# Kernel tuning notes

Hardware: AMD Instinct MI355X
Metric: run time of the kernel (lower is better)

## Reference

```python
import jax, jax.numpy as jnp
import numpy as np

RELU_NEG_SLOPE = 0.2

def _gat_layer(x, W, a, src, dst, num_nodes, concat):
    # x: [N, Din]; W: [H, Din, F]; a: [H, 2F]; src/dst: [E]
    H, _, F = W.shape
    proj = jnp.einsum('nd,hdf->nhf', x, W)              # [N, H, F]
    a_self, a_nb = a[:, :F], a[:, F:]                   # [H, F] each
    alpha_self = jnp.einsum('nhf,hf->nh', proj, a_self) # [N, H]
    alpha_nb = jnp.einsum('nhf,hf->nh', proj, a_nb)     # [N, H]
    # edge score: a . [proj_dst || proj_src], dst = center node i, src = neighbor j
    e = jax.nn.leaky_relu(alpha_self[dst] + alpha_nb[src], RELU_NEG_SLOPE)  # [E, H]
    e_max = jax.ops.segment_max(e, dst, num_segments=num_nodes)
    e_exp = jnp.exp(e - e_max[dst])
    denom = jax.ops.segment_sum(e_exp, dst, num_segments=num_nodes)
    w = e_exp / denom[dst]                              # [E, H] softmax per dst node
    msg = proj[src] * w[:, :, None]                     # [E, H, F]
    out = jax.ops.segment_sum(msg, dst, num_segments=num_nodes)  # [N, H, F]
    if concat:
        return out.reshape(num_nodes, H * F)
    return out.mean(axis=1)


def setup_inputs() -> dict:
    key = jax.random.key(0)
    k1, k2, k3, k4, k5, k6 = jax.random.split(key, 6)
    N, Din, F1, H1 = 10000, 128, 64, 8
    Dmid = H1 * F1  # 512
    F2, H2 = 64, 1
    x = jax.random.normal(k1, (N, Din), dtype=jnp.float32)
    edges = jax.random.randint(k2, (2, 80000), 0, N, dtype=jnp.int64)
    W1 = jax.random.normal(k3, (H1, Din, F1), dtype=jnp.float32) / np.sqrt(Din)
    a1 = jax.random.normal(k4, (H1, 2 * F1), dtype=jnp.float32) / np.sqrt(2 * F1)
    W2 = jax.random.normal(k5, (H2, Dmid, F2), dtype=jnp.float32) / np.sqrt(Dmid)
    a2 = jax.random.normal(k6, (H2, 2 * F2), dtype=jnp.float32) / np.sqrt(2 * F2)
    return {"x": x, "edges": edges, "W1": W1, "a1": a1, "W2": W2, "a2": a2}


def reference(x, edges, W1, a1, W2, a2):
    N = x.shape[0]
    loops = jnp.arange(N, dtype=edges.dtype)
    # undirected graph + self loops (Graph.neighborhood adds both directions and self)
    src = jnp.concatenate([edges[0], edges[1], loops])
    dst = jnp.concatenate([edges[1], edges[0], loops])
    h = _gat_layer(x, W1, a1, src, dst, N, concat=True)   # [N, 512]
    h = jax.nn.elu(h)
    out = _gat_layer(h, W2, a2, src, dst, N, concat=False)  # [N, 64]
    return out
```

## Files before the change

kernel.cpp:

```cpp
#include <hip/hip_runtime.h>
#include <hip/hip_bf16.h>
#include <hip/hip_fp16.h>

#define RELU_NEG_SLOPE 0.2f

typedef _Float16 half8 __attribute__((ext_vector_type(8)));
typedef float f32x4 __attribute__((ext_vector_type(4)));

__device__ __forceinline__ float leaky(float e) {
    return (e > 0.f) ? e : RELU_NEG_SLOPE * e;
}

__device__ __forceinline__ float elu1(float x) {
    return (x > 0.f) ? x : (__expf(x) - 1.f);
}

__global__ __launch_bounds__(256) void stage_kernel(
    const float4* __restrict__ x4, const float* __restrict__ W1,
    const float* __restrict__ W2, float2* __restrict__ xh,
    __half* __restrict__ Bt1, __half* __restrict__ W2t,
    int* __restrict__ cnt, int n4, int t1, int t2, int N) {
    int i = blockIdx.x * 256 + threadIdx.x;
    if (i < n4) {
        float4 v = x4[i];
        float2 p;
        ((__half2*)&p)[0] = __floats2half2_rn(v.x, v.y);
        ((__half2*)&p)[1] = __floats2half2_rn(v.z, v.w);
        xh[i] = p;
    } else if (i < n4 + t1) {
        int j = i - n4;
        int f = j & 63;
        int d = (j >> 6) & 127;
        int h = j >> 13;
        Bt1[((h * 64 + f) << 7) + d] = __float2half(W1[j]);
    } else if (i < n4 + t1 + t2) {
        int j = i - n4 - t1;
        int f = j & 63;
        int d = j >> 6;
        W2t[f * 512 + d] = __float2half(W2[j]);
    } else if (i < n4 + t1 + t2 + N) {
        cnt[i - n4 - t1 - t2] = 0;
    }
}

__global__ __launch_bounds__(256) void scatter_gemm1(
    const int* __restrict__ edges, int E0, int* __restrict__ cnt,
    unsigned short* __restrict__ ell, int nscat,
    const __half* __restrict__ Ah, const __half* __restrict__ Bt,
    const float* __restrict__ a1, __half* __restrict__ Cp,
    float* __restrict__ as_, float* __restrict__ an_, int M, int slabN) {
    if (blockIdx.x < nscat) {
        int i = blockIdx.x * 256 + threadIdx.x;
        if (i >= 2 * E0) return;
        int s = edges[i];
        int d = (i < E0) ? edges[E0 + i] : edges[i - E0];
        int pos = atomicAdd(&cnt[d], 1);
        ell[(d << 6) + pos] = (unsigned short)s;
        return;
    }
    int bid2 = blockIdx.x - nscat;
    const int h = bid2 & 7;
    const int by = bid2 >> 3;
    const int lane = threadIdx.x & 63;
    const int wave = threadIdx.x >> 6;
    const int q = lane >> 4;
    const int l15 = lane & 15;
    const int mrow = by * 64 + wave * 16;

    f32x4 acc[4] = {{0.f, 0.f, 0.f, 0.f}, {0.f, 0.f, 0.f, 0.f},
                    {0.f, 0.f, 0.f, 0.f}, {0.f, 0.f, 0.f, 0.f}};
    const __half* Ap = Ah + (size_t)(mrow + l15) * 128 + q * 8;
    const __half* Bp = Bt + (size_t)(h * 64 + l15) * 128 + q * 8;
#pragma unroll
    for (int ks = 0; ks < 4; ks++) {
        half8 av = *(const half8*)(Ap + ks * 32);
#pragma unroll
        for (int t = 0; t < 4; t++) {
            half8 bv = *(const half8*)(Bp + (size_t)t * 16 * 128 + ks * 32);
            acc[t] = __builtin_amdgcn_mfma_f32_16x16x32_f16(av, bv, acc[t], 0, 0, 0);
        }
    }

    __half* Cs = Cp + (size_t)(h >> 1) * slabN + (h & 1) * 64;
    float asc[4], anc[4];
#pragma unroll
    for (int t = 0; t < 4; t++) {
        asc[t] = a1[h * 128 + t * 16 + l15];
        anc[t] = a1[h * 128 + 64 + t * 16 + l15];
    }
#pragma unroll
    for (int r = 0; r < 4; r++) {
        int mg = mrow + q * 4 + r;
        float ps = 0.f, pn = 0.f;
#pragma unroll
        for (int t = 0; t < 4; t++) {
            float v = acc[t][r];
            ps += v * asc[t];
            pn += v * anc[t];
            if (mg < M)
                Cs[(size_t)mg * 128 + t * 16 + l15] = __float2half(v);
        }
#pragma unroll
        for (int m = 8; m >= 1; m >>= 1) {
            ps += __shfl_xor(ps, m, 64);
            pn += __shfl_xor(pn, m, 64);
        }
        if (l15 == 0 && mg < M) {
            as_[mg * 8 + h] = ps;
            an_[mg * 8 + h] = pn;
        }
    }
}

__global__ __launch_bounds__(256) void agg_h8_sliced(
    const int* __restrict__ cnt, const unsigned short* __restrict__ ell,
    const __half* __restrict__ projp, const float* __restrict__ as_,
    const float* __restrict__ an_, __half* __restrict__ outh,
    int N, int slabN) {
    int bid = blockIdx.x;
    int hp = bid & 3;
    int rem = bid >> 2;
    int d = rem * 4 + (threadIdx.x >> 6);
    int lane = threadIdx.x & 63;
    if (d >= N) return;
    const int sub = lane >> 3;
    const int inner = lane & 7;
    const int hh = inner >> 2;
    const int h = hp * 2 + hh;
    const int c16 = (inner & 3) * 16;

    int deg = cnt[d];
    const unsigned short* row = ell + (d << 6);
    float asd = as_[d * 8 + h];
    const __half* slab = projp + (size_t)hp * slabN;

    float acc[16];
#pragma unroll
    for (int i = 0; i < 16; i++) acc[i] = 0.f;
    float den = 0.f;
    if (sub == 0) {
        float e = __expf(leaky(asd + an_[d * 8 + h]));
        const __half* p = slab + (size_t)d * 128 + hh * 64 + c16;
        half8 v0 = *(const half8*)p;
        half8 v1 = *(const half8*)(p + 8);
        den = e;
#pragma unroll
        for (int i = 0; i < 8; i++) {
            acc[i] = e * (float)v0[i];
            acc[8 + i] = e * (float)v1[i];
        }
    }
    for (int j0 = 0; j0 < deg; j0 += 8) {
        int j = j0 + sub;
        int jc = (j < deg) ? j : (deg - 1);
        int s = row[jc];
        float e = __expf(leaky(asd + an_[s * 8 + h]));
        if (j >= deg) e = 0.f;
        const __half* p = slab + (size_t)s * 128 + hh * 64 + c16;
        half8 v0 = *(const half8*)p;
        half8 v1 = *(const half8*)(p + 8);
        den += e;
#pragma unroll
        for (int i = 0; i < 8; i++) {
            acc[i] += e * (float)v0[i];
            acc[8 + i] += e * (float)v1[i];
        }
    }

#pragma unroll
    for (int off = 32; off >= 8; off >>= 1) {
#pragma unroll
        for (int i = 0; i < 16; i++) acc[i] += __shfl_down(acc[i], off, 64);
        den += __shfl_down(den, off, 64);
    }

    if (sub == 0) {
        float r = 1.f / den;
        half8 o0, o1;
#pragma unroll
        for (int i = 0; i < 8; i++) {
            o0[i] = (_Float16)elu1(acc[i] * r);
            o1[i] = (_Float16)elu1(acc[8 + i] * r);
        }
        __half* op = outh + (size_t)d * 512 + h * 64 + c16;
        *(half8*)op = o0;
        *(half8*)(op + 8) = o1;
    }
}

__global__ __launch_bounds__(64) void mfma_gemm2(
    const __half* __restrict__ Ah, const __half* __restrict__ Bt,
    const float* __restrict__ a2, __half* __restrict__ Ch,
    float* __restrict__ as_, float* __restrict__ an_, int M) {
    const int lane = threadIdx.x & 63;
    const int q = lane >> 4;
    const int l15 = lane & 15;
    const int mrow = blockIdx.x * 16;

    f32x4 acc[4] = {{0.f, 0.f, 0.f, 0.f}, {0.f, 0.f, 0.f, 0.f},
                    {0.f, 0.f, 0.f, 0.f}, {0.f, 0.f, 0.f, 0.f}};
    const __half* Ap = Ah + (size_t)(mrow + l15) * 512 + q * 8;
    const __half* Bp = Bt + (size_t)l15 * 512 + q * 8;
#pragma unroll
    for (int ks = 0; ks < 16; ks++) {
        half8 av = *(const half8*)(Ap + ks * 32);
#pragma unroll
        for (int t = 0; t < 4; t++) {
            half8 bv = *(const half8*)(Bp + (size_t)t * 16 * 512 + ks * 32);
            acc[t] = __builtin_amdgcn_mfma_f32_16x16x32_f16(av, bv, acc[t], 0, 0, 0);
        }
    }

    float asc[4], anc[4];
#pragma unroll
    for (int t = 0; t < 4; t++) {
        asc[t] = a2[t * 16 + l15];
        anc[t] = a2[64 + t * 16 + l15];
    }
#pragma unroll
    for (int r = 0; r < 4; r++) {
        int mg = mrow + q * 4 + r;
        float ps = 0.f, pn = 0.f;
#pragma unroll
        for (int t = 0; t < 4; t++) {
            float v = acc[t][r];
            ps += v * asc[t];
            pn += v * anc[t];
            if (mg < M)
                Ch[(size_t)mg * 64 + t * 16 + l15] = __float2half(v);
        }
#pragma unroll
        for (int m = 8; m >= 1; m >>= 1) {
            ps += __shfl_xor(ps, m, 64);
            pn += __shfl_xor(pn, m, 64);
        }
        if (l15 == 0 && mg < M) {
            as_[mg] = ps;
            an_[mg] = pn;
        }
    }
}

__global__ __launch_bounds__(256) void agg_node_h1(
    const int* __restrict__ cnt, const unsigned short* __restrict__ ell,
    const __half* __restrict__ projh, const float* __restrict__ as_,
    const float* __restrict__ an_, float* __restrict__ out, int N) {
    int d = blockIdx.x * 4 + (threadIdx.x >> 6);
    int lane = threadIdx.x & 63;
    if (d >= N) return;
    int sub = lane >> 3;
    int inner = lane & 7;
    int deg = cnt[d];
    const unsigned short* row = ell + (d << 6);
    float asd = as_[d];

    float acc[8];
#pragma unroll
    for (int i = 0; i < 8; i++) acc[i] = 0.f;
    float den = 0.f;
    for (int j0 = 0; j0 < deg; j0 += 8) {
        int j = j0 + sub;
        int jc = (j < deg) ? j : (deg - 1);
        int s = row[jc];
        float e = __expf(leaky(asd + an_[s]));
        if (j >= deg) e = 0.f;
        half8 v = *(const half8*)(projh + (size_t)s * 64 + inner * 8);
        den += e;
#pragma unroll
        for (int i = 0; i < 8; i++) acc[i] += e * (float)v[i];
    }

#pragma unroll
    for (int off = 32; off >= 8; off >>= 1) {
#pragma unroll
        for (int i = 0; i < 8; i++) acc[i] += __shfl_down(acc[i], off, 64);
        den += __shfl_down(den, off, 64);
    }

    if (sub == 0) {
        float e = __expf(leaky(asd + an_[d]));
        half8 v = *(const half8*)(projh + (size_t)d * 64 + inner * 8);
        den += e;
#pragma unroll
        for (int i = 0; i < 8; i++) acc[i] += e * (float)v[i];
        float rden = 1.f / den;
        float4 r0, r1;
        r0.x = acc[0] * rden; r0.y = acc[1] * rden;
        r0.z = acc[2] * rden; r0.w = acc[3] * rden;
        r1.x = acc[4] * rden; r1.y = acc[5] * rden;
        r1.z = acc[6] * rden; r1.w = acc[7] * rden;
        float* op = out + (size_t)d * 64 + inner * 8;
        *(float4*)op = r0;
        *(float4*)(op + 4) = r1;
    }
}

extern "C" void kernel_launch(void* const* d_in, const int* in_sizes, int n_in,
                              void* d_out, int out_size, void* d_ws, size_t ws_size,
                              hipStream_t stream) {
    const float* x  = (const float*)d_in[0];
    const int* edges = (const int*)d_in[1];
    const float* W1 = (const float*)d_in[2];
    const float* a1 = (const float*)d_in[3];
    const float* W2 = (const float*)d_in[4];
    const float* a2 = (const float*)d_in[5];

    const int Din = 128, H1 = 8, F = 64, Dmid = 512;
    const int N = in_sizes[0] / Din;
    const int E0 = in_sizes[1] / 2;
    const int Mpad = (N + 63) & ~63;
    const int slabN = Mpad * 128;

    char* base = (char*)d_ws;
    size_t off = 0;
    auto take = [&](size_t bytes) {
        void* p = base + off;
        off = (off + bytes + 255) & ~(size_t)255;
        return p;
    };
    __half* x_h    = (__half*)take((size_t)Mpad * Din * 2);
    __half* proj1p = (__half*)take((size_t)4 * slabN * 2);
    __half* hbufh  = (__half*)take((size_t)Mpad * Dmid * 2);
    __half* proj2h = (__half*)take((size_t)N * F * 2);
    __half* Bt1    = (__half*)take((size_t)Dmid * Din * 2);
    __half* W2t    = (__half*)take((size_t)F * Dmid * 2);
    float* as1 = (float*)take((size_t)N * H1 * 4);
    float* an1 = (float*)take((size_t)N * H1 * 4);
    float* as2 = (float*)take((size_t)N * 4);
    float* an2 = (float*)take((size_t)N * 4);
    int* cnt = (int*)take((size_t)N * 4);
    unsigned short* ell = (unsigned short*)take((size_t)N * 64 * 2);

    int n4 = N * Din / 4;
    int t1 = H1 * Din * F, t2 = Dmid * F;
    int total = n4 + t1 + t2 + N;
    stage_kernel<<<(total + 255) / 256, 256, 0, stream>>>(
        (const float4*)x, W1, W2, (float2*)x_h, Bt1, W2t, cnt, n4, t1, t2, N);

    int nscat = (2 * E0 + 255) / 256;
    int ngemm = H1 * ((N + 63) / 64);
    scatter_gemm1<<<nscat + ngemm, 256, 0, stream>>>(
        edges, E0, cnt, ell, nscat,
        x_h, Bt1, a1, proj1p, as1, an1, N, slabN);

    int nbp = (N + 3) / 4;
    agg_h8_sliced<<<4 * nbp, 256, 0, stream>>>(cnt, ell, proj1p, as1, an1,
                                               hbufh, N, slabN);

    mfma_gemm2<<<(N + 15) / 16, 64, 0, stream>>>(hbufh, W2t, a2, proj2h,
                                                 as2, an2, N);

    agg_node_h1<<<(N + 3) / 4, 256, 0, stream>>>(cnt, ell, proj2h,
                                                 as2, an2, (float*)d_out, N);
}
```

Before: 140.9 us.

## Fuse all GAT stages into one cooperative persistent kernel with grid syncs

Merges the five separate kernel launches (stage, scatter+gemm1, agg1, gemm2, agg2) into one cooperative persistent kernel. The stages are separated by grid-wide barriers, and each stage's work is distributed with grid-stride loops over blocks or waves. The aim is to remove per-launch overhead and the gaps between kernels. In exchange, occupancy is capped at a fixed grid size of up to 1024 blocks, grid syncs have their own cost, and the standalone kernels remain as a fallback if the cooperative launch fails.

Result: slower. 439.6 us (+211.9%).

```diff
diff --git a/kernel.cpp b/kernel.cpp
--- a/kernel.cpp
+++ b/kernel.cpp
@@ -1,6 +1,8 @@
 #include <hip/hip_runtime.h>
-#include <hip/hip_bf16.h>
 #include <hip/hip_fp16.h>
+#include <hip/hip_cooperative_groups.h>
+
+namespace cg = cooperative_groups;
 
 #define RELU_NEG_SLOPE 0.2f
 
@@ -15,62 +17,68 @@
     return (x > 0.f) ? x : (__expf(x) - 1.f);
 }
 
-__global__ __launch_bounds__(256) void stage_kernel(
-    const float4* __restrict__ x4, const float* __restrict__ W1,
-    const float* __restrict__ W2, float2* __restrict__ xh,
-    __half* __restrict__ Bt1, __half* __restrict__ W2t,
-    int* __restrict__ cnt, int n4, int t1, int t2, int N) {
-    int i = blockIdx.x * 256 + threadIdx.x;
-    if (i < n4) {
-        float4 v = x4[i];
-        float2 p;
-        ((__half2*)&p)[0] = __floats2half2_rn(v.x, v.y);
-        ((__half2*)&p)[1] = __floats2half2_rn(v.z, v.w);
-        xh[i] = p;
-    } else if (i < n4 + t1) {
-        int j = i - n4;
+struct GatParams {
+    const float4* __restrict__ x4;
+    const float* __restrict__ W1;
+    const float* __restrict__ W2;
+    const float* __restrict__ a1;
+    const float* __restrict__ a2;
+    const int* __restrict__ edges;
+    float2* __restrict__ xh;
+    __half* __restrict__ Bt1;
+    __half* __restrict__ W2t;
+    int* __restrict__ cnt;
+    unsigned short* __restrict__ ell;
+    __half* __restrict__ proj1p;
+    float* __restrict__ as1;
+    float* __restrict__ an1;
+    __half* __restrict__ hbufh;
+    __half* __restrict__ proj2h;
+    float* __restrict__ as2;
+    float* __restrict__ an2;
+    float* __restrict__ out;
+    int N, E0, n4, t1, t2, slabN, ntiles1, ntiles2;
+};
+
+
+__device__ __forceinline__ void stage_item(const GatParams& p, int i) {
+    if (i < p.n4) {
+        float4 v = p.x4[i];
+        float2 o;
+        ((__half2*)&o)[0] = __floats2half2_rn(v.x, v.y);
+        ((__half2*)&o)[1] = __floats2half2_rn(v.z, v.w);
+        p.xh[i] = o;
+    } else if (i < p.n4 + p.t1) {
+        int j = i - p.n4;
         int f = j & 63;
         int d = (j >> 6) & 127;
         int h = j >> 13;
-        Bt1[((h * 64 + f) << 7) + d] = __float2half(W1[j]);
-    } else if (i < n4 + t1 + t2) {
-        int j = i - n4 - t1;
+        p.Bt1[((h * 64 + f) << 7) + d] = __float2half(p.W1[j]);
+    } else if (i < p.n4 + p.t1 + p.t2) {
+        int j = i - p.n4 - p.t1;
         int f = j & 63;
         int d = j >> 6;
-        W2t[f * 512 + d] = __float2half(W2[j]);
-    } else if (i < n4 + t1 + t2 + N) {
-        cnt[i - n4 - t1 - t2] = 0;
-    }
-}
-
-__global__ __launch_bounds__(256) void scatter_gemm1(
-    const int* __restrict__ edges, int E0, int* __restrict__ cnt,
-    unsigned short* __restrict__ ell, int nscat,
-    const __half* __restrict__ Ah, const __half* __restrict__ Bt,
-    const float* __restrict__ a1, __half* __restrict__ Cp,
-    float* __restrict__ as_, float* __restrict__ an_, int M, int slabN) {
-    if (blockIdx.x < nscat) {
-        int i = blockIdx.x * 256 + threadIdx.x;
-        if (i >= 2 * E0) return;
-        int s = edges[i];
-        int d = (i < E0) ? edges[E0 + i] : edges[i - E0];
-        int pos = atomicAdd(&cnt[d], 1);
-        ell[(d << 6) + pos] = (unsigned short)s;
-        return;
-    }
-    int bid2 = blockIdx.x - nscat;
-    const int h = bid2 & 7;
-    const int by = bid2 >> 3;
-    const int lane = threadIdx.x & 63;
-    const int wave = threadIdx.x >> 6;
+        p.W2t[f * 512 + d] = __float2half(p.W2[j]);
+    } else {
+        p.cnt[i - p.n4 - p.t1 - p.t2] = 0;
+    }
+}
+
+__device__ __forceinline__ void scatter_item(const GatParams& p, int i) {
+    int s = p.edges[i];
+    int d = (i < p.E0) ? p.edges[p.E0 + i] : p.edges[i - p.E0];
+    int pos = atomicAdd(&p.cnt[d], 1);
+    p.ell[(d << 6) + pos] = (unsigned short)s;
+}
+
+__device__ __forceinline__ void gemm1_wave(const GatParams& p, int h,
+                                           int mrow, int lane) {
     const int q = lane >> 4;
     const int l15 = lane & 15;
-    const int mrow = by * 64 + wave * 16;
-
     f32x4 acc[4] = {{0.f, 0.f, 0.f, 0.f}, {0.f, 0.f, 0.f, 0.f},
                     {0.f, 0.f, 0.f, 0.f}, {0.f, 0.f, 0.f, 0.f}};
-    const __half* Ap = Ah + (size_t)(mrow + l15) * 128 + q * 8;
-    const __half* Bp = Bt + (size_t)(h * 64 + l15) * 128 + q * 8;
+    const __half* Ap = (const __half*)p.xh + (size_t)(mrow + l15) * 128 + q * 8;
+    const __half* Bp = p.Bt1 + (size_t)(h * 64 + l15) * 128 + q * 8;
 #pragma unroll
     for (int ks = 0; ks < 4; ks++) {
         half8 av = *(const half8*)(Ap + ks * 32);
@@ -80,13 +88,12 @@
             acc[t] = __builtin_amdgcn_mfma_f32_16x16x32_f16(av, bv, acc[t], 0, 0, 0);
         }
     }
-
-    __half* Cs = Cp + (size_t)(h >> 1) * slabN + (h & 1) * 64;
+    __half* Cs = p.proj1p + (size_t)(h >> 1) * p.slabN + (h & 1) * 64;
     float asc[4], anc[4];
 #pragma unroll
     for (int t = 0; t < 4; t++) {
-        asc[t] = a1[h * 128 + t * 16 + l15];
-        anc[t] = a1[h * 128 + 64 + t * 16 + l15];
+        asc[t] = p.a1[h * 128 + t * 16 + l15];
+        anc[t] = p.a1[h * 128 + 64 + t * 16 + l15];
     }
 #pragma unroll
     for (int r = 0; r < 4; r++) {
@@ -97,7 +104,7 @@
             float v = acc[t][r];
             ps += v * asc[t];
             pn += v * anc[t];
-            if (mg < M)
+            if (mg < p.N)
                 Cs[(size_t)mg * 128 + t * 16 + l15] = __float2half(v);
         }
 #pragma unroll
@@ -105,44 +112,35 @@
             ps += __shfl_xor(ps, m, 64);
             pn += __shfl_xor(pn, m, 64);
         }
-        if (l15 == 0 && mg < M) {
-            as_[mg * 8 + h] = ps;
-            an_[mg * 8 + h] = pn;
-        }
-    }
-}
-
-__global__ __launch_bounds__(256) void agg_h8_sliced(
-    const int* __restrict__ cnt, const unsigned short* __restrict__ ell,
-    const __half* __restrict__ projp, const float* __restrict__ as_,
-    const float* __restrict__ an_, __half* __restrict__ outh,
-    int N, int slabN) {
-    int bid = blockIdx.x;
-    int hp = bid & 3;
-    int rem = bid >> 2;
-    int d = rem * 4 + (threadIdx.x >> 6);
-    int lane = threadIdx.x & 63;
-    if (d >= N) return;
+        if (l15 == 0 && mg < p.N) {
+            p.as1[mg * 8 + h] = ps;
+            p.an1[mg * 8 + h] = pn;
+        }
+    }
+}
+
+__device__ __forceinline__ void aggh8_wave(const GatParams& p, int hp, int d,
+                                           int lane) {
     const int sub = lane >> 3;
     const int inner = lane & 7;
     const int hh = inner >> 2;
     const int h = hp * 2 + hh;
     const int c16 = (inner & 3) * 16;
 
-    int deg = cnt[d];
-    const unsigned short* row = ell + (d << 6);
-    float asd = as_[d * 8 + h];
-    const __half* slab = projp + (size_t)hp * slabN;
+    int deg = p.cnt[d];
+    const unsigned short* row = p.ell + (d << 6);
+    float asd = p.as1[d * 8 + h];
+    const __half* slab = p.proj1p + (size_t)hp * p.slabN;
 
     float acc[16];
 #pragma unroll
     for (int i = 0; i < 16; i++) acc[i] = 0.f;
     float den = 0.f;
     if (sub == 0) {
-        float e = __expf(leaky(asd + an_[d * 8 + h]));
-        const __half* p = slab + (size_t)d * 128 + hh * 64 + c16;
-        half8 v0 = *(const half8*)p;
-        half8 v1 = *(const half8*)(p + 8);
+        float e = __expf(leaky(asd + p.an1[d * 8 + h]));
+        const __half* q = slab + (size_t)d * 128 + hh * 64 + c16;
+        half8 v0 = *(const half8*)q;
+        half8 v1 = *(const half8*)(q + 8);
         den = e;
 #pragma unroll
         for (int i = 0; i < 8; i++) {
@@ -154,11 +152,11 @@
         int j = j0 + sub;
         int jc = (j < deg) ? j : (deg - 1);
         int s = row[jc];
-        float e = __expf(leaky(asd + an_[s * 8 + h]));
+        float e = __expf(leaky(asd + p.an1[s * 8 + h]));
         if (j >= deg) e = 0.f;
-        const __half* p = slab + (size_t)s * 128 + hh * 64 + c16;
-        half8 v0 = *(const half8*)p;
-        half8 v1 = *(const half8*)(p + 8);
+        const __half* q = slab + (size_t)s * 128 + hh * 64 + c16;
+        half8 v0 = *(const half8*)q;
+        half8 v1 = *(const half8*)(q + 8);
         den += e;
 #pragma unroll
         for (int i = 0; i < 8; i++) {
@@ -166,14 +164,12 @@
             acc[8 + i] += e * (float)v1[i];
         }
     }
-
 #pragma unroll
     for (int off = 32; off >= 8; off >>= 1) {
 #pragma unroll
         for (int i = 0; i < 16; i++) acc[i] += __shfl_down(acc[i], off, 64);
         den += __shfl_down(den, off, 64);
     }
-
     if (sub == 0) {
         float r = 1.f / den;
         half8 o0, o1;
@@ -182,25 +178,20 @@
             o0[i] = (_Float16)elu1(acc[i] * r);
             o1[i] = (_Float16)elu1(acc[8 + i] * r);
         }
-        __half* op = outh + (size_t)d * 512 + h * 64 + c16;
+        __half* op = p.hbufh + (size_t)d * 512 + h * 64 + c16;
         *(half8*)op = o0;
         *(half8*)(op + 8) = o1;
     }
 }
 
-__global__ __launch_bounds__(64) void mfma_gemm2(
-    const __half* __restrict__ Ah, const __half* __restrict__ Bt,
-    const float* __restrict__ a2, __half* __restrict__ Ch,
-    float* __restrict__ as_, float* __restrict__ an_, int M) {
-    const int lane = threadIdx.x & 63;
+__device__ __forceinline__ void gemm2_wave(const GatParams& p, int mrow,
+                                           int lane) {
     const int q = lane >> 4;
     const int l15 = lane & 15;
-    const int mrow = blockIdx.x * 16;
-
     f32x4 acc[4] = {{0.f, 0.f, 0.f, 0.f}, {0.f, 0.f, 0.f, 0.f},
                     {0.f, 0.f, 0.f, 0.f}, {0.f, 0.f, 0.f, 0.f}};
-    const __half* Ap = Ah + (size_t)(mrow + l15) * 512 + q * 8;
-    const __half* Bp = Bt + (size_t)l15 * 512 + q * 8;
+    const __half* Ap = p.hbufh + (size_t)(mrow + l15) * 512 + q * 8;
+    const __half* Bp = p.W2t + (size_t)l15 * 512 + q * 8;
 #pragma unroll
     for (int ks = 0; ks < 16; ks++) {
         half8 av = *(const half8*)(Ap + ks * 32);
@@ -210,12 +201,11 @@
             acc[t] = __builtin_amdgcn_mfma_f32_16x16x32_f16(av, bv, acc[t], 0, 0, 0);
         }
     }
-
     float asc[4], anc[4];
 #pragma unroll
     for (int t = 0; t < 4; t++) {
-        asc[t] = a2[t * 16 + l15];
-        anc[t] = a2[64 + t * 16 + l15];
+        asc[t] = p.a2[t * 16 + l15];
+        anc[t] = p.a2[64 + t * 16 + l15];
     }
 #pragma unroll
     for (int r = 0; r < 4; r++) {
@@ -226,33 +216,28 @@
             float v = acc[t][r];
             ps += v * asc[t];
             pn += v * anc[t];
-            if (mg < M)
-                Ch[(size_t)mg * 64 + t * 16 + l15] = __float2half(v);
+            if (mg < p.N)
+                p.proj2h[(size_t)mg * 64 + t * 16 + l15] = __float2half(v);
         }
 #pragma unroll
         for (int m = 8; m >= 1; m >>= 1) {
             ps += __shfl_xor(ps, m, 64);
             pn += __shfl_xor(pn, m, 64);
         }
-        if (l15 == 0 && mg < M) {
-            as_[mg] = ps;
-            an_[mg] = pn;
-        }
-    }
-}
-
-__global__ __launch_bounds__(256) void agg_node_h1(
-    const int* __restrict__ cnt, const unsigned short* __restrict__ ell,
-    const __half* __restrict__ projh, const float* __restrict__ as_,
-    const float* __restrict__ an_, float* __restrict__ out, int N) {
-    int d = blockIdx.x * 4 + (threadIdx.x >> 6);
-    int lane = threadIdx.x & 63;
-    if (d >= N) return;
+        if (l15 == 0 && mg < p.N) {
+            p.as2[mg] = ps;
+            p.an2[mg] = pn;
+        }
+    }
+}
+
+__device__ __forceinline__ void aggnode_wave(const GatParams& p, int d,
+                                             int lane) {
     int sub = lane >> 3;
     int inner = lane & 7;
-    int deg = cnt[d];
-    const unsigned short* row = ell + (d << 6);
-    float asd = as_[d];
+    int deg = p.cnt[d];
+    const unsigned short* row = p.ell + (d << 6);
+    float asd = p.as2[d];
 
     float acc[8];
 #pragma unroll
@@ -262,24 +247,22 @@
         int j = j0 + sub;
         int jc = (j < deg) ? j : (deg - 1);
         int s = row[jc];
-        float e = __expf(leaky(asd + an_[s]));
+        float e = __expf(leaky(asd + p.an2[s]));
         if (j >= deg) e = 0.f;
-        half8 v = *(const half8*)(projh + (size_t)s * 64 + inner * 8);
+        half8 v = *(const half8*)(p.proj2h + (size_t)s * 64 + inner * 8);
         den += e;
 #pragma unroll
         for (int i = 0; i < 8; i++) acc[i] += e * (float)v[i];
     }
-
 #pragma unroll
     for (int off = 32; off >= 8; off >>= 1) {
 #pragma unroll
         for (int i = 0; i < 8; i++) acc[i] += __shfl_down(acc[i], off, 64);
         den += __shfl_down(den, off, 64);
     }
-
     if (sub == 0) {
-        float e = __expf(leaky(asd + an_[d]));
-        half8 v = *(const half8*)(projh + (size_t)d * 64 + inner * 8);
+        float e = __expf(leaky(asd + p.an2[d]));
+        half8 v = *(const half8*)(p.proj2h + (size_t)d * 64 + inner * 8);
         den += e;
 #pragma unroll
         for (int i = 0; i < 8; i++) acc[i] += e * (float)v[i];
@@ -289,22 +272,85 @@
         r0.z = acc[2] * rden; r0.w = acc[3] * rden;
         r1.x = acc[4] * rden; r1.y = acc[5] * rden;
         r1.z = acc[6] * rden; r1.w = acc[7] * rden;
-        float* op = out + (size_t)d * 64 + inner * 8;
+        float* op = p.out + (size_t)d * 64 + inner * 8;
         *(float4*)op = r0;
         *(float4*)(op + 4) = r1;
     }
+}
+
+__global__ __launch_bounds__(256, 4) void gat_fused(GatParams p) {
+    cg::grid_group gg = cg::this_grid();
+    const int bid = blockIdx.x;
+    const int tid = threadIdx.x;
+    const int nb = gridDim.x;
+    const int gsz = nb * 256;
+    const int wave = tid >> 6;
+    const int lane = tid & 63;
+    const int gw = bid * 4 + wave;
+    const int nwv = nb * 4;
+
+    {
+        int total = p.n4 + p.t1 + p.t2 + p.N;
+        for (int i = bid * 256 + tid; i < total; i += gsz) stage_item(p, i);
+    }
+    gg.sync();
+
+    {
+        int tot = 2 * p.E0;
+        for (int i = bid * 256 + tid; i < tot; i += gsz) scatter_item(p, i);
+        for (int t = gw; t < p.ntiles1; t += nwv)
+            gemm1_wave(p, t & 7, (t >> 3) << 4, lane);
+    }
+    gg.sync();
+
+    {
+        int hp = bid & 3;
+        for (int d = (bid >> 2) * 4 + wave; d < p.N; d += nb)
+            aggh8_wave(p, hp, d, lane);
+    }
+    gg.sync();
+
+    for (int t = gw; t < p.ntiles2; t += nwv) gemm2_wave(p, t << 4, lane);
+    gg.sync();
+
+    for (int d = gw; d < p.N; d += nwv) aggnode_wave(p, d, lane);
+}
+
+__global__ __launch_bounds__(256) void k_stage(GatParams p) {
+    int i = blockIdx.x * 256 + threadIdx.x;
+    int total = p.n4 + p.t1 + p.t2 + p.N;
+    if (i < total) stage_item(p, i);
+}
+
+__global__ __launch_bounds__(256) void k_scatter_gemm1(GatParams p, int nscat) {
+    if (blockIdx.x < nscat) {
+        int i = blockIdx.x * 256 + threadIdx.x;
+        if (i < 2 * p.E0) scatter_item(p, i);
+        return;
+    }
+    int bid2 = blockIdx.x - nscat;
+    gemm1_wave(p, bid2 & 7, (bid2 >> 3) * 64 + (threadIdx.x >> 6) * 16,
+               threadIdx.x & 63);
+}
+
+__global__ __launch_bounds__(256) void k_agg1(GatParams p) {
+    int bid = blockIdx.x;
+    int d = (bid >> 2) * 4 + (threadIdx.x >> 6);
+    if (d < p.N) aggh8_wave(p, bid & 3, d, threadIdx.x & 63);
+}
+
+__global__ __launch_bounds__(64) void k_gemm2(GatParams p) {
+    gemm2_wave(p, blockIdx.x * 16, threadIdx.x & 63);
+}
+
+__global__ __launch_bounds__(256) void k_agg2(GatParams p) {
+    int d = blockIdx.x * 4 + (threadIdx.x >> 6);
+    if (d < p.N) aggnode_wave(p, d, threadIdx.x & 63);
 }
 
 extern "C" void kernel_launch(void* const* d_in, const int* in_sizes, int n_in,
                               void* d_out, int out_size, void* d_ws, size_t ws_size,
                               hipStream_t stream) {
-    const float* x  = (const float*)d_in[0];
-    const int* edges = (const int*)d_in[1];
-    const float* W1 = (const float*)d_in[2];
-    const float* a1 = (const float*)d_in[3];
-    const float* W2 = (const float*)d_in[4];
-    const float* a2 = (const float*)d_in[5];
-
     const int Din = 128, H1 = 8, F = 64, Dmid = 512;
     const int N = in_sizes[0] / Din;
     const int E0 = in_sizes[1] / 2;
@@ -314,9 +360,9 @@
     char* base = (char*)d_ws;
     size_t off = 0;
     auto take = [&](size_t bytes) {
-        void* p = base + off;
+        void* q = base + off;
         off = (off + bytes + 255) & ~(size_t)255;
-        return p;
+        return q;
     };
     __half* x_h    = (__half*)take((size_t)Mpad * Din * 2);
     __half* proj1p = (__half*)take((size_t)4 * slabN * 2);
@@ -331,25 +377,58 @@
     int* cnt = (int*)take((size_t)N * 4);
     unsigned short* ell = (unsigned short*)take((size_t)N * 64 * 2);
 
-    int n4 = N * Din / 4;
-    int t1 = H1 * Din * F, t2 = Dmid * F;
-    int total = n4 + t1 + t2 + N;
-    stage_kernel<<<(total + 255) / 256, 256, 0, stream>>>(
-        (const float4*)x, W1, W2, (float2*)x_h, Bt1, W2t, cnt, n4, t1, t2, N);
-
+    GatParams p;
+    p.x4 = (const float4*)d_in[0];
+    p.edges = (const int*)d_in[1];
+    p.W1 = (const float*)d_in[2];
+    p.a1 = (const float*)d_in[3];
+    p.W2 = (const float*)d_in[4];
+    p.a2 = (const float*)d_in[5];
+    p.xh = (float2*)x_h;
+    p.Bt1 = Bt1; p.W2t = W2t; p.cnt = cnt; p.ell = ell;
+    p.proj1p = proj1p; p.as1 = as1; p.an1 = an1;
+    p.hbufh = hbufh; p.proj2h = proj2h; p.as2 = as2; p.an2 = an2;
+    p.out = (float*)d_out;
+    p.N = N; p.E0 = E0;
+    p.n4 = N * Din / 4;
+    p.t1 = H1 * Din * F;
+    p.t2 = Dmid * F;
+    p.slabN = slabN;
+    p.ntiles1 = 8 * (Mpad >> 4);
+    p.ntiles2 = (N + 15) >> 4;
+
+    static int coop_state = -1;
+    if (coop_state != 0) {
+        static int grid_blocks = -1;
+        if (grid_blocks < 0) {
+            int nbcu = 0;
+            if (hipOccupancyMaxActiveBlocksPerMultiprocessor(
+                    &nbcu, (const void*)gat_fused, 256, 0) != hipSuccess)
+                nbcu = 0;
+            int g = nbcu * 256;
+            if (g > 1024) g = 1024;
+            g &= ~7;
+            grid_blocks = g;
+        }
+        if (grid_blocks >= 8) {
+            void* args[] = {(void*)&p};
+            hipError_t e = hipLaunchCooperativeKernel(
+                (const void*)gat_fused, dim3(grid_blocks), dim3(256), args, 0,
+                stream);
+            if (e == hipSuccess) {
+                coop_state = 1;
+                return;
+            }
+        }
+        coop_state = 0;
+    }
+
+    int total = p.n4 + p.t1 + p.t2 + N;
+    k_stage<<<(total + 255) / 256, 256, 0, stream>>>(p);
     int nscat = (2 * E0 + 255) / 256;
     int ngemm = H1 * ((N + 63) / 64);
-    scatter_gemm1<<<nscat + ngemm, 256, 0, stream>>>(
-        edges, E0, cnt, ell, nscat,
-        x_h, Bt1, a1, proj1p, as1, an1, N, slabN);
-
-    int nbp = (N + 3) / 4;
-    agg_h8_sliced<<<4 * nbp, 256, 0, stream>>>(cnt, ell, proj1p, as1, an1,
-                                               hbufh, N, slabN);
-
-    mfma_gemm2<<<(N + 15) / 16, 64, 0, stream>>>(hbufh, W2t, a2, proj2h,
-                                                 as2, an2, N);
-
-    agg_node_h1<<<(N + 3) / 4, 256, 0, stream>>>(cnt, ell, proj2h,
-                                                 as2, an2, (float*)d_out, N);
-}
+    k_scatter_gemm1<<<nscat + ngemm, 256, 0, stream>>>(p, nscat);
+    k_agg1<<<4 * ((N + 3) / 4), 256, 0, stream>>>(p);
+    k_gemm2<<<(N + 15) / 16, 64, 0, stream>>>(p);
+    k_agg2<<<(N + 3) / 4, 256, 0, stream>>>(p);
+}
```

## Fuse staging kernel into scatter/GEMM1 and reset degree counts in final kernel

Applied to the files above, without the earlier changes.

Removes the separate staging kernel. The fp32 x rows are now converted to fp16 inside the GEMM1 waves, and each block transposes its W1 head slice into shared memory. The W2 transpose moves into the scatter blocks. Degree counters now live in a global device array that the final aggregation kernel zeroes after reading, so the counts are cleared for the next call instead of by a memset-like pass. This saves one launch and the fp16 staging round-trip, but every GEMM block redundantly re-transposes W1, and correctness depends on the prior call having reset g_cnt (the very first call depends on static zero-initialisation).

After: 133.4 us. -5.4%, faster.

```diff
diff --git a/kernel.cpp b/kernel.cpp
--- a/kernel.cpp
+++ b/kernel.cpp
@@ -1,5 +1,4 @@
 #include <hip/hip_runtime.h>
-#include <hip/hip_bf16.h>
 #include <hip/hip_fp16.h>
 
 #define RELU_NEG_SLOPE 0.2f
@@ -15,68 +14,76 @@
     return (x > 0.f) ? x : (__expf(x) - 1.f);
 }
 
-__global__ __launch_bounds__(256) void stage_kernel(
+__device__ int g_cnt[16384];
+
+__global__ __launch_bounds__(256) void k1_scatter_gemm1(
+    const int* __restrict__ edges, int E0,
+    const float* __restrict__ W2, __half* __restrict__ W2t, int t2,
+    unsigned short* __restrict__ ell, int nscat,
     const float4* __restrict__ x4, const float* __restrict__ W1,
-    const float* __restrict__ W2, float2* __restrict__ xh,
-    __half* __restrict__ Bt1, __half* __restrict__ W2t,
-    int* __restrict__ cnt, int n4, int t1, int t2, int N) {
-    int i = blockIdx.x * 256 + threadIdx.x;
-    if (i < n4) {
-        float4 v = x4[i];
-        float2 p;
-        ((__half2*)&p)[0] = __floats2half2_rn(v.x, v.y);
-        ((__half2*)&p)[1] = __floats2half2_rn(v.z, v.w);
-        xh[i] = p;
-    } else if (i < n4 + t1) {
-        int j = i - n4;
-        int f = j & 63;
-        int d = (j >> 6) & 127;
-        int h = j >> 13;
-        Bt1[((h * 64 + f) << 7) + d] = __float2half(W1[j]);
-    } else if (i < n4 + t1 + t2) {
-        int j = i - n4 - t1;
-        int f = j & 63;
-        int d = j >> 6;
-        W2t[f * 512 + d] = __float2half(W2[j]);
-    } else if (i < n4 + t1 + t2 + N) {
-        cnt[i - n4 - t1 - t2] = 0;
-    }
-}
-
-__global__ __launch_bounds__(256) void scatter_gemm1(
-    const int* __restrict__ edges, int E0, int* __restrict__ cnt,
-    unsigned short* __restrict__ ell, int nscat,
-    const __half* __restrict__ Ah, const __half* __restrict__ Bt,
     const float* __restrict__ a1, __half* __restrict__ Cp,
-    float* __restrict__ as_, float* __restrict__ an_, int M, int slabN) {
+    float* __restrict__ as_, float* __restrict__ an_, int N, int slabN) {
+    __shared__ __half Bs[64 * 132];
     if (blockIdx.x < nscat) {
         int i = blockIdx.x * 256 + threadIdx.x;
-        if (i >= 2 * E0) return;
-        int s = edges[i];
-        int d = (i < E0) ? edges[E0 + i] : edges[i - E0];
-        int pos = atomicAdd(&cnt[d], 1);
-        ell[(d << 6) + pos] = (unsigned short)s;
+        if (i < 2 * E0) {
+            int s = edges[i];
+            int d = (i < E0) ? edges[E0 + i] : edges[i - E0];
+            int pos = atomicAdd(&g_cnt[d], 1);
+            ell[(d << 6) + pos] = (unsigned short)s;
+        } else if (i < 2 * E0 + t2) {
+            int j = i - 2 * E0;
+            int f = j & 63;
+            int d = j >> 6;
+            W2t[f * 512 + d] = __float2half(W2[j]);
+        }
         return;
     }
     int bid2 = blockIdx.x - nscat;
     const int h = bid2 & 7;
     const int by = bid2 >> 3;
+
+    {
+        const float4* W1h = (const float4*)W1 + h * 2048;
+        int t = threadIdx.x;
+#pragma unroll
+        for (int r = 0; r < 8; r++) {
+            int j4 = t + r * 256;
+            float4 w = W1h[j4];
+            int f = (j4 << 2) & 63;
+            int d = j4 >> 4;
+            Bs[(f + 0) * 132 + d] = __float2half(w.x);
+            Bs[(f + 1) * 132 + d] = __float2half(w.y);
+            Bs[(f + 2) * 132 + d] = __float2half(w.z);
+            Bs[(f + 3) * 132 + d] = __float2half(w.w);
+        }
+    }
+    __syncthreads();
+
     const int lane = threadIdx.x & 63;
     const int wave = threadIdx.x >> 6;
     const int q = lane >> 4;
     const int l15 = lane & 15;
     const int mrow = by * 64 + wave * 16;
 
+    int arow = mrow + l15;
+    if (arow >= N) arow = N - 1;
+    const float4* Ar = x4 + (size_t)arow * 32;
+
     f32x4 acc[4] = {{0.f, 0.f, 0.f, 0.f}, {0.f, 0.f, 0.f, 0.f},
                     {0.f, 0.f, 0.f, 0.f}, {0.f, 0.f, 0.f, 0.f}};
-    const __half* Ap = Ah + (size_t)(mrow + l15) * 128 + q * 8;
-    const __half* Bp = Bt + (size_t)(h * 64 + l15) * 128 + q * 8;
 #pragma unroll
     for (int ks = 0; ks < 4; ks++) {
-        half8 av = *(const half8*)(Ap + ks * 32);
+        float4 a0 = Ar[ks * 8 + q * 2];
+        float4 a1v = Ar[ks * 8 + q * 2 + 1];
+        half8 av;
+        av[0] = (_Float16)a0.x; av[1] = (_Float16)a0.y;
+        av[2] = (_Float16)a0.z; av[3] = (_Float16)a0.w;
+        av[4] = (_Float16)a1v.x; av[5] = (_Float16)a1v.y;
+        av[6] = (_Float16)a1v.z; av[7] = (_Float16)a1v.w;
 #pragma unroll
         for (int t = 0; t < 4; t++) {
-            half8 bv = *(const half8*)(Bp + (size_t)t * 16 * 128 + ks * 32);
+            half8 bv = *(const half8*)(Bs + (t * 16 + l15) * 132 + q * 8 + ks * 32);
             acc[t] = __builtin_amdgcn_mfma_f32_16x16x32_f16(av, bv, acc[t], 0, 0, 0);
         }
     }
@@ -97,7 +104,7 @@
             float v = acc[t][r];
             ps += v * asc[t];
             pn += v * anc[t];
-            if (mg < M)
+            if (mg < N)
                 Cs[(size_t)mg * 128 + t * 16 + l15] = __float2half(v);
         }
 #pragma unroll
@@ -105,7 +112,7 @@
             ps += __shfl_xor(ps, m, 64);
             pn += __shfl_xor(pn, m, 64);
         }
-        if (l15 == 0 && mg < M) {
+        if (l15 == 0 && mg < N) {
             as_[mg * 8 + h] = ps;
             an_[mg * 8 + h] = pn;
         }
@@ -113,7 +120,7 @@
 }
 
 __global__ __launch_bounds__(256) void agg_h8_sliced(
-    const int* __restrict__ cnt, const unsigned short* __restrict__ ell,
+    const unsigned short* __restrict__ ell,
     const __half* __restrict__ projp, const float* __restrict__ as_,
     const float* __restrict__ an_, __half* __restrict__ outh,
     int N, int slabN) {
@@ -129,7 +136,7 @@
     const int h = hp * 2 + hh;
     const int c16 = (inner & 3) * 16;
 
-    int deg = cnt[d];
+    int deg = g_cnt[d];
     const unsigned short* row = ell + (d << 6);
     float asd = as_[d * 8 + h];
     const __half* slab = projp + (size_t)hp * slabN;
@@ -242,7 +249,7 @@
 }
 
 __global__ __launch_bounds__(256) void agg_node_h1(
-    const int* __restrict__ cnt, const unsigned short* __restrict__ ell,
+    const unsigned short* __restrict__ ell,
     const __half* __restrict__ projh, const float* __restrict__ as_,
     const float* __restrict__ an_, float* __restrict__ out, int N) {
     int d = blockIdx.x * 4 + (threadIdx.x >> 6);
@@ -250,7 +257,8 @@
     if (d >= N) return;
     int sub = lane >> 3;
     int inner = lane & 7;
-    int deg = cnt[d];
+    int deg = g_cnt[d];
+    if (lane == 0) g_cnt[d] = 0;
     const unsigned short* row = ell + (d << 6);
     float asd = as_[d];
 
@@ -318,38 +326,30 @@
         off = (off + bytes + 255) & ~(size_t)255;
         return p;
     };
-    __half* x_h    = (__half*)take((size_t)Mpad * Din * 2);
     __half* proj1p = (__half*)take((size_t)4 * slabN * 2);
     __half* hbufh  = (__half*)take((size_t)Mpad * Dmid * 2);
     __half* proj2h = (__half*)take((size_t)N * F * 2);
-    __half* Bt1    = (__half*)take((size_t)Dmid * Din * 2);
     __half* W2t    = (__half*)take((size_t)F * Dmid * 2);
     float* as1 = (float*)take((size_t)N * H1 * 4);
     float* an1 = (float*)take((size_t)N * H1 * 4);
     float* as2 = (float*)take((size_t)N * 4);
     float* an2 = (float*)take((size_t)N * 4);
-    int* cnt = (int*)take((size_t)N * 4);
     unsigned short* ell = (unsigned short*)take((size_t)N * 64 * 2);
 
-    int n4 = N * Din / 4;
-    int t1 = H1 * Din * F, t2 = Dmid * F;
-    int total = n4 + t1 + t2 + N;
-    stage_kernel<<<(total + 255) / 256, 256, 0, stream>>>(
-        (const float4*)x, W1, W2, (float2*)x_h, Bt1, W2t, cnt, n4, t1, t2, N);
-
-    int nscat = (2 * E0 + 255) / 256;
-    int ngemm = H1 * ((N + 63) / 64);
-    scatter_gemm1<<<nscat + ngemm, 256, 0, stream>>>(
-        edges, E0, cnt, ell, nscat,
-        x_h, Bt1, a1, proj1p, as1, an1, N, slabN);
+    int t2 = Dmid * F;
+    int nscat = (2 * E0 + t2 + 255) / 256;
+    int ngemm = H1 * (Mpad / 64);
+    k1_scatter_gemm1<<<nscat + ngemm, 256, 0, stream>>>(
+        edges, E0, W2, W2t, t2, ell, nscat,
+        (const float4*)x, W1, a1, proj1p, as1, an1, N, slabN);
 
     int nbp = (N + 3) / 4;
-    agg_h8_sliced<<<4 * nbp, 256, 0, stream>>>(cnt, ell, proj1p, as1, an1,
+    agg_h8_sliced<<<4 * nbp, 256, 0, stream>>>(ell, proj1p, as1, an1,
                                                hbufh, N, slabN);
 
     mfma_gemm2<<<(N + 15) / 16, 64, 0, stream>>>(hbufh, W2t, a2, proj2h,
                                                  as2, an2, N);
 
-    agg_node_h1<<<(N + 3) / 4, 256, 0, stream>>>(cnt, ell, proj2h,
+    agg_node_h1<<<(N + 3) / 4, 256, 0, stream>>>(ell, proj2h,
                                                  as2, an2, (float*)d_out, N);
 }
```
